# Performance work log

Measured on AMD Instinct MI355X. Metric: run time of the kernel, lower is better.

## Reference

```python
import jax, jax.numpy as jnp
import numpy as np

B, S, D, H = 4, 2048, 1024, 16
HD = D // H  # head_dim = 64


def setup_inputs() -> dict:
    key = jax.random.key(0)
    k1, k2, k3 = jax.random.split(key, 3)
    scale = 0.02
    return {
        "hidden_states": jax.random.normal(k1, (B, S, D), dtype=jnp.float32),
        "W_attn": jax.random.normal(k2, (D, 3 * D), dtype=jnp.float32) * scale,
        "b_attn": jnp.zeros((3 * D,), dtype=jnp.float32),
        "W_proj": jax.random.normal(k3, (D, D), dtype=jnp.float32) * scale,
        "b_proj": jnp.zeros((D,), dtype=jnp.float32),
    }


def reference(hidden_states, W_attn, b_attn, W_proj, b_proj):
    b, s, d = hidden_states.shape
    qkv = hidden_states @ W_attn + b_attn  # [B,S,3D]
    q, k, v = jnp.split(qkv, 3, axis=-1)
    # [B,S,D] -> [B,H,S,hd]
    def to_heads(x):
        return x.reshape(b, s, H, HD).transpose(0, 2, 1, 3)
    q, k, v = to_heads(q), to_heads(k), to_heads(v)
    scores = jnp.einsum("bhqd,bhkd->bhqk", q, k) / jnp.sqrt(jnp.float32(HD))
    causal = jnp.tril(jnp.ones((s, s), dtype=bool))  # [S,S]
    scores = jnp.where(causal[None, None], scores, jnp.float32(-jnp.inf))
    probs = jax.nn.softmax(scores, axis=-1)  # dropout p=0 -> identity (eval)
    out = jnp.einsum("bhqk,bhkd->bhqd", probs, v)  # [B,H,S,hd]
    out = out.transpose(0, 2, 1, 3).reshape(b, s, d)
    return out @ W_proj + b_proj
```

## Files before the change

kernel.cpp:

```cpp
#include <hip/hip_runtime.h>
#include <hip/hip_bf16.h>


typedef float f32x4 __attribute__((ext_vector_type(4)));
typedef __bf16 bf16x8 __attribute__((ext_vector_type(8)));
typedef unsigned short u16x8 __attribute__((ext_vector_type(8)));
typedef unsigned short u16x4 __attribute__((ext_vector_type(4)));

static constexpr int Sq = 2048, Dm = 1024, HD = 64, N3 = 3072;
static constexpr int Mrows = 4 * Sq;
static constexpr float SM_SCALE = 0.18033688011112042f;
static constexpr float SM_BIAS  = -11.541560327111707f;

__device__ __forceinline__ unsigned short f2bf(float f) {
  return __builtin_bit_cast(unsigned short, (__bf16)f);
}
__device__ __forceinline__ f32x4 mfma16(u16x8 a, u16x8 b, f32x4 c) {
  return __builtin_amdgcn_mfma_f32_16x16x32_bf16(
      __builtin_bit_cast(bf16x8, a), __builtin_bit_cast(bf16x8, b), c, 0, 0, 0);
}

__global__ __launch_bounds__(256) void cvt_k(
    const float* __restrict__ in, unsigned short* __restrict__ out, int n) {
  int stride = gridDim.x * 256 * 4;
  for (int i = (blockIdx.x * 256 + threadIdx.x) * 4; i < n; i += stride) {
    f32x4 v = *reinterpret_cast<const f32x4*>(&in[i]);
    u16x4 o;
    #pragma unroll
    for (int j = 0; j < 4; j++) o[j] = f2bf(v[j]);
    *reinterpret_cast<u16x4*>(&out[i]) = o;
  }
}

__global__ __launch_bounds__(256) void tcvt_k(
    const float* __restrict__ in, unsigned short* __restrict__ out,
    int R, int C) {
  __shared__ float tile[32][33];
  int c0 = blockIdx.x * 32, r0 = blockIdx.y * 32;
  int tx = threadIdx.x & 31, ty = threadIdx.x >> 5;
  #pragma unroll
  for (int i = 0; i < 32; i += 8)
    tile[ty + i][tx] = in[(size_t)(r0 + ty + i) * C + c0 + tx];
  __syncthreads();
  #pragma unroll
  for (int i = 0; i < 32; i += 8)
    out[(size_t)(c0 + ty + i) * R + r0 + tx] = f2bf(tile[tx][ty + i]);
}

template <bool OUT_F32>
__global__ __launch_bounds__(256) void gemm_bt(
    const unsigned short* __restrict__ A, const unsigned short* __restrict__ Bt,
    const float* __restrict__ bias, void* __restrict__ Cout,
    int Md, int Nd, int Kd) {
  __shared__ unsigned short Asm[128 * 32];
  __shared__ unsigned short Bsm[128 * 32];
  int t = threadIdx.x;
  int wave = t >> 6, lane = t & 63;
  int lrow = lane & 15, lq = lane >> 4;
  int wr = wave >> 1, wc = wave & 1;
  int bm = blockIdx.y * 128, bn = blockIdx.x * 128;
  f32x4 acc[4][4] = {};

  for (int k0 = 0; k0 < Kd; k0 += 32) {
    __syncthreads();
    #pragma unroll
    for (int c = 0; c < 2; c++) {
      int e = c * 2048 + t * 8;
      int row = e >> 5, col = e & 31;
      const unsigned short* ga = A + (size_t)(bm + row) * Kd + k0 + col;
      const unsigned short* gb = Bt + (size_t)(bn + row) * Kd + k0 + col;
      __builtin_amdgcn_global_load_lds(
          (const __attribute__((address_space(1))) void*)ga,
          (__attribute__((address_space(3))) void*)((char*)Asm + c * 4096 + wave * 1024),
          16, 0, 0);
      __builtin_amdgcn_global_load_lds(
          (const __attribute__((address_space(1))) void*)gb,
          (__attribute__((address_space(3))) void*)((char*)Bsm + c * 4096 + wave * 1024),
          16, 0, 0);
    }
    __syncthreads();

    u16x8 af[4], bfr[4];
    #pragma unroll
    for (int m = 0; m < 4; m++)
      af[m] = *reinterpret_cast<const u16x8*>(&Asm[(wr * 64 + m * 16 + lrow) * 32 + lq * 8]);
    #pragma unroll
    for (int n = 0; n < 4; n++)
      bfr[n] = *reinterpret_cast<const u16x8*>(&Bsm[(wc * 64 + n * 16 + lrow) * 32 + lq * 8]);
    #pragma unroll
    for (int m = 0; m < 4; m++)
      #pragma unroll
      for (int n = 0; n < 4; n++)
        acc[m][n] = mfma16(af[m], bfr[n], acc[m][n]);
  }

  #pragma unroll
  for (int n = 0; n < 4; n++) {
    int col = bn + wc * 64 + n * 16 + lrow;
    float bv = bias[col];
    #pragma unroll
    for (int m = 0; m < 4; m++) {
      #pragma unroll
      for (int j = 0; j < 4; j++) {
        int row = bm + wr * 64 + m * 16 + lq * 4 + j;
        if constexpr (OUT_F32)
          ((float*)Cout)[(size_t)row * Nd + col] = acc[m][n][j] + bv;
        else
          ((unsigned short*)Cout)[(size_t)row * Nd + col] = f2bf(acc[m][n][j] + bv);
      }
    }
  }
}

__global__ __launch_bounds__(256) void attn_k(
    const unsigned short* __restrict__ qkv,
    unsigned short* __restrict__ ao) {
  int bh = blockIdx.y;
  int b = bh >> 4, h = bh & 15;
  int t = threadIdx.x, wave = t >> 6, lane = t & 63;
  int lrow = lane & 15, lq = lane >> 4;

  __shared__ unsigned short Kl[2][64][72];
  __shared__ unsigned short Vt[2][64][72];
  __shared__ unsigned short Pl[4][16][72];

  const size_t base = (size_t)b * Sq * N3;
  const unsigned short* Kbase = qkv + base + Dm + h * HD;
  const unsigned short* Vbase = qkv + base + 2 * Dm + h * HD;

  int irow = t >> 2, icol = (t & 3) * 16;
  int vd = lane, vkb = wave;

  u16x8 kr0, kr1, vr0, vr1;
  auto prefetch = [&](int kv) {
    const unsigned short* kp = Kbase + (size_t)(kv + irow) * N3 + icol;
    kr0 = *reinterpret_cast<const u16x8*>(kp);
    kr1 = *reinterpret_cast<const u16x8*>(kp + 8);
    const unsigned short* vp = Vbase + (size_t)kv * N3 + vd;
    #pragma unroll
    for (int i = 0; i < 8; i++) {
      vr0[i] = vp[(size_t)(vkb * 8 + i) * N3];
      vr1[i] = vp[(size_t)(32 + vkb * 8 + i) * N3];
    }
  };

  #pragma unroll 1
  for (int pass = 0; pass < 2; ++pass) {
    int qb = pass ? (int)blockIdx.x : 15 - (int)blockIdx.x;
    int q0 = qb * 128;
    int ntiles = 2 * qb + 2;

    u16x8 qf[2][2];
    #pragma unroll
    for (int m = 0; m < 2; m++) {
      const unsigned short* qp =
          qkv + base + (size_t)(q0 + wave * 32 + m * 16 + lrow) * N3 + h * HD + lq * 8;
      qf[m][0] = *reinterpret_cast<const u16x8*>(qp);
      qf[m][1] = *reinterpret_cast<const u16x8*>(qp + 32);
    }

    float lrun[2][4] = {};
    f32x4 oacc[2][4] = {};

    prefetch(0);

    #pragma unroll 1
    for (int kt = 0; kt < ntiles; ++kt) {
      int kv = kt * 64, bsel = kt & 1;
      *reinterpret_cast<u16x8*>(&Kl[bsel][irow][icol]) = kr0;
      *reinterpret_cast<u16x8*>(&Kl[bsel][irow][icol + 8]) = kr1;
      *reinterpret_cast<u16x8*>(&Vt[bsel][vd][vkb * 8]) = vr0;
      *reinterpret_cast<u16x8*>(&Vt[bsel][vd][32 + vkb * 8]) = vr1;
      if (kt + 1 < ntiles) prefetch(kv + 64);
      __syncthreads();

      u16x8 kf0[4], kf1[4], vf0[4], vf1[4];
      #pragma unroll
      for (int ct = 0; ct < 4; ct++) {
        kf0[ct] = *reinterpret_cast<const u16x8*>(&Kl[bsel][ct * 16 + lrow][lq * 8]);
        kf1[ct] = *reinterpret_cast<const u16x8*>(&Kl[bsel][ct * 16 + lrow][32 + lq * 8]);
      }
      f32x4 sacc[2][4] = {};
      #pragma unroll
      for (int m = 0; m < 2; m++)
        #pragma unroll
        for (int ct = 0; ct < 4; ct++) {
          sacc[m][ct] = mfma16(qf[m][0], kf0[ct], sacc[m][ct]);
          sacc[m][ct] = mfma16(qf[m][1], kf1[ct], sacc[m][ct]);
        }
      #pragma unroll
      for (int ht = 0; ht < 4; ht++) {
        vf0[ht] = *reinterpret_cast<const u16x8*>(&Vt[bsel][ht * 16 + lrow][lq * 8]);
        vf1[ht] = *reinterpret_cast<const u16x8*>(&Vt[bsel][ht * 16 + lrow][32 + lq * 8]);
      }

      #pragma unroll
      for (int m = 0; m < 2; m++) {
        int rbase = q0 + wave * 32 + m * 16 + lq * 4;
        float p[4][4], rs[4] = {0.f, 0.f, 0.f, 0.f};
        #pragma unroll
        for (int ct = 0; ct < 4; ct++) {
          int colg = kv + ct * 16 + lrow;
          #pragma unroll
          for (int j = 0; j < 4; j++) {
            float e = exp2f(fmaf(sacc[m][ct][j], SM_SCALE, SM_BIAS));
            e = (colg <= rbase + j) ? e : 0.f;
            p[ct][j] = e;
            rs[j] += e;
          }
        }
        #pragma unroll
        for (int j = 0; j < 4; j++) {
          rs[j] += __shfl_xor(rs[j], 1);
          rs[j] += __shfl_xor(rs[j], 2);
          rs[j] += __shfl_xor(rs[j], 4);
          rs[j] += __shfl_xor(rs[j], 8);
          lrun[m][j] += rs[j];
        }

        #pragma unroll
        for (int ct = 0; ct < 4; ct++)
          #pragma unroll
          for (int j = 0; j < 4; j++)
            Pl[wave][lq * 4 + j][ct * 16 + lrow] = f2bf(p[ct][j]);

        u16x8 pa0 = *reinterpret_cast<const u16x8*>(&Pl[wave][lrow][lq * 8]);
        u16x8 pa1 = *reinterpret_cast<const u16x8*>(&Pl[wave][lrow][32 + lq * 8]);
        #pragma unroll
        for (int ht = 0; ht < 4; ht++) {
          oacc[m][ht] = mfma16(pa0, vf0[ht], oacc[m][ht]);
          oacc[m][ht] = mfma16(pa1, vf1[ht], oacc[m][ht]);
        }
      }
    }

    #pragma unroll
    for (int m = 0; m < 2; m++)
      #pragma unroll
      for (int ht = 0; ht < 4; ht++)
        #pragma unroll
        for (int j = 0; j < 4; j++) {
          int rg = q0 + wave * 32 + m * 16 + lq * 4 + j;
          float v = oacc[m][ht][j] / lrun[m][j];
          ao[(size_t)(b * Sq + rg) * Dm + h * HD + ht * 16 + lrow] = f2bf(v);
        }
  }
}

extern "C" void kernel_launch(void* const* d_in, const int* in_sizes, int n_in,
                              void* d_out, int out_size, void* d_ws, size_t ws_size,
                              hipStream_t stream) {
  const float* hs = (const float*)d_in[0];
  const float* Wa = (const float*)d_in[1];
  const float* ba = (const float*)d_in[2];
  const float* Wp = (const float*)d_in[3];
  const float* bp = (const float*)d_in[4];
  float* out = (float*)d_out;

  char* ws = (char*)d_ws;
  unsigned short* QKV = (unsigned short*)ws;
  unsigned short* WaT = (unsigned short*)(ws + 50331648);
  unsigned short* AO  = (unsigned short*)(ws + 50331648);
  unsigned short* WpT = (unsigned short*)ws;
  unsigned short* hsB = (unsigned short*)d_out;

  cvt_k<<<2048, 256, 0, stream>>>(hs, hsB, Mrows * Dm);
  tcvt_k<<<dim3(96, 32), 256, 0, stream>>>(Wa, WaT, 1024, 3072);
  gemm_bt<false><<<dim3(24, 64), 256, 0, stream>>>(hsB, WaT, ba, QKV, Mrows, N3, Dm);
  attn_k<<<dim3(8, 64), 256, 0, stream>>>(QKV, AO);
  tcvt_k<<<dim3(32, 32), 256, 0, stream>>>(Wp, WpT, 1024, 1024);
  gemm_bt<true><<<dim3(8, 64), 256, 0, stream>>>(AO, WpT, bp, out, Mrows, Dm, Dm);
}
```

Measured before the change: 232.9 us.

## Swizzle V-transpose LDS layout, defer row-sum shuffles, skip mask on full tiles

Three changes to the attention inner loop. An XOR swizzle on the transposed V tile in LDS is meant to cut bank conflicts on both the per-lane stores and the MFMA fragment reads. Row-sum lane shuffles move out of the key-tile loop: each lane keeps a partial sum and reduces once per pass. The causal mask compare is skipped for tiles lying entirely below the diagonal. Together these cut per-iteration shuffle and ALU work, at the cost of more complex LDS indexing.

After: 227.3 us. 2.4% less time.

```diff
diff --git a/kernel.cpp b/kernel.cpp
--- a/kernel.cpp
+++ b/kernel.cpp
@@ -130,6 +130,7 @@
 
   int irow = t >> 2, icol = (t & 3) * 16;
   int vd = lane, vkb = wave;
+  int vswW = ((vd >> 3) & 7) << 3;
 
   u16x8 kr0, kr1, vr0, vr1;
   auto prefetch = [&](int kv) {
@@ -169,8 +170,8 @@
       int kv = kt * 64, bsel = kt & 1;
       *reinterpret_cast<u16x8*>(&Kl[bsel][irow][icol]) = kr0;
       *reinterpret_cast<u16x8*>(&Kl[bsel][irow][icol + 8]) = kr1;
-      *reinterpret_cast<u16x8*>(&Vt[bsel][vd][vkb * 8]) = vr0;
-      *reinterpret_cast<u16x8*>(&Vt[bsel][vd][32 + vkb * 8]) = vr1;
+      *reinterpret_cast<u16x8*>(&Vt[bsel][vd][(vkb * 8) ^ vswW]) = vr0;
+      *reinterpret_cast<u16x8*>(&Vt[bsel][vd][(32 + vkb * 8) ^ vswW]) = vr1;
       if (kt + 1 < ntiles) prefetch(kv + 64);
       __syncthreads();
 
@@ -190,32 +191,27 @@
         }
       #pragma unroll
       for (int ht = 0; ht < 4; ht++) {
-        vf0[ht] = *reinterpret_cast<const u16x8*>(&Vt[bsel][ht * 16 + lrow][lq * 8]);
-        vf1[ht] = *reinterpret_cast<const u16x8*>(&Vt[bsel][ht * 16 + lrow][32 + lq * 8]);
+        int vsw = ((2 * ht + (lrow >> 3)) & 7) << 3;
+        vf0[ht] = *reinterpret_cast<const u16x8*>(&Vt[bsel][ht * 16 + lrow][(lq * 8) ^ vsw]);
+        vf1[ht] = *reinterpret_cast<const u16x8*>(&Vt[bsel][ht * 16 + lrow][(32 + lq * 8) ^ vsw]);
       }
 
       #pragma unroll
       for (int m = 0; m < 2; m++) {
-        int rbase = q0 + wave * 32 + m * 16 + lq * 4;
-        float p[4][4], rs[4] = {0.f, 0.f, 0.f, 0.f};
+        int rwm = q0 + wave * 32 + m * 16;
+        int rbase = rwm + lq * 4;
+        bool need_mask = kv + 63 > rwm;
+        float p[4][4];
         #pragma unroll
         for (int ct = 0; ct < 4; ct++) {
           int colg = kv + ct * 16 + lrow;
           #pragma unroll
           for (int j = 0; j < 4; j++) {
             float e = exp2f(fmaf(sacc[m][ct][j], SM_SCALE, SM_BIAS));
-            e = (colg <= rbase + j) ? e : 0.f;
+            if (need_mask) e = (colg <= rbase + j) ? e : 0.f;
             p[ct][j] = e;
-            rs[j] += e;
+            lrun[m][j] += e;
           }
-        }
-        #pragma unroll
-        for (int j = 0; j < 4; j++) {
-          rs[j] += __shfl_xor(rs[j], 1);
-          rs[j] += __shfl_xor(rs[j], 2);
-          rs[j] += __shfl_xor(rs[j], 4);
-          rs[j] += __shfl_xor(rs[j], 8);
-          lrun[m][j] += rs[j];
         }
 
         #pragma unroll
@@ -233,6 +229,18 @@
         }
       }
     }
+
+    #pragma unroll
+    for (int m = 0; m < 2; m++)
+      #pragma unroll
+      for (int j = 0; j < 4; j++) {
+        float r = lrun[m][j];
+        r += __shfl_xor(r, 1);
+        r += __shfl_xor(r, 2);
+        r += __shfl_xor(r, 4);
+        r += __shfl_xor(r, 8);
+        lrun[m][j] = r;
+      }
 
     #pragma unroll
     for (int m = 0; m < 2; m++)
```

## Transpose QK^T MFMA operands to keep row sums lane-local and vectorize P stores

Applied to the files above, without the earlier changes.

Swaps the A/B operands of the score MFMA so each lane holds scores for a single query row. The per-tile row-sum shuffles become one cross-lane reduction after the KV loop, and P can be written to LDS as packed 4-element vectors instead of scattered scalars. The causal mask is now applied only on tiles that cross the diagonal, and the final division uses a fast reciprocal. The layout change must stay consistent with the P/V MFMA, and the reciprocal is slightly less accurate.

Result: faster. 212.9 us (-8.6%).

```diff
diff --git a/kernel.cpp b/kernel.cpp
--- a/kernel.cpp
+++ b/kernel.cpp
@@ -159,7 +159,7 @@
       qf[m][1] = *reinterpret_cast<const u16x8*>(qp + 32);
     }
 
-    float lrun[2][4] = {};
+    float lrun[2] = {0.f, 0.f};
     f32x4 oacc[2][4] = {};
 
     prefetch(0);
@@ -185,8 +185,8 @@
       for (int m = 0; m < 2; m++)
         #pragma unroll
         for (int ct = 0; ct < 4; ct++) {
-          sacc[m][ct] = mfma16(qf[m][0], kf0[ct], sacc[m][ct]);
-          sacc[m][ct] = mfma16(qf[m][1], kf1[ct], sacc[m][ct]);
+          sacc[m][ct] = mfma16(kf0[ct], qf[m][0], sacc[m][ct]);
+          sacc[m][ct] = mfma16(kf1[ct], qf[m][1], sacc[m][ct]);
         }
       #pragma unroll
       for (int ht = 0; ht < 4; ht++) {
@@ -196,33 +196,28 @@
 
       #pragma unroll
       for (int m = 0; m < 2; m++) {
-        int rbase = q0 + wave * 32 + m * 16 + lq * 4;
-        float p[4][4], rs[4] = {0.f, 0.f, 0.f, 0.f};
+        int rwm = q0 + wave * 32 + m * 16;
+        bool need_mask = kv + 63 > rwm;
+        int dlim = rwm - kv + lrow;
+        float p[4][4];
         #pragma unroll
         for (int ct = 0; ct < 4; ct++) {
-          int colg = kv + ct * 16 + lrow;
           #pragma unroll
           for (int j = 0; j < 4; j++) {
             float e = exp2f(fmaf(sacc[m][ct][j], SM_SCALE, SM_BIAS));
-            e = (colg <= rbase + j) ? e : 0.f;
+            if (need_mask) e = (16 * ct + 4 * lq + j <= dlim) ? e : 0.f;
             p[ct][j] = e;
-            rs[j] += e;
+            lrun[m] += e;
           }
         }
-        #pragma unroll
-        for (int j = 0; j < 4; j++) {
-          rs[j] += __shfl_xor(rs[j], 1);
-          rs[j] += __shfl_xor(rs[j], 2);
-          rs[j] += __shfl_xor(rs[j], 4);
-          rs[j] += __shfl_xor(rs[j], 8);
-          lrun[m][j] += rs[j];
-        }
-
-        #pragma unroll
-        for (int ct = 0; ct < 4; ct++)
+
+        #pragma unroll
+        for (int ct = 0; ct < 4; ct++) {
+          u16x4 o;
           #pragma unroll
-          for (int j = 0; j < 4; j++)
-            Pl[wave][lq * 4 + j][ct * 16 + lrow] = f2bf(p[ct][j]);
+          for (int j = 0; j < 4; j++) o[j] = f2bf(p[ct][j]);
+          *reinterpret_cast<u16x4*>(&Pl[wave][lrow][16 * ct + 4 * lq]) = o;
+        }
 
         u16x8 pa0 = *reinterpret_cast<const u16x8*>(&Pl[wave][lrow][lq * 8]);
         u16x8 pa1 = *reinterpret_cast<const u16x8*>(&Pl[wave][lrow][32 + lq * 8]);
@@ -235,15 +230,28 @@
     }
 
     #pragma unroll
-    for (int m = 0; m < 2; m++)
+    for (int m = 0; m < 2; m++) {
+      float r = lrun[m];
+      r += __shfl_xor(r, 16);
+      r += __shfl_xor(r, 32);
+      lrun[m] = r;
+    }
+
+    #pragma unroll
+    for (int m = 0; m < 2; m++) {
+      float inv[4];
+      #pragma unroll
+      for (int j = 0; j < 4; j++)
+        inv[j] = __builtin_amdgcn_rcpf(__shfl(lrun[m], lq * 4 + j));
       #pragma unroll
       for (int ht = 0; ht < 4; ht++)
         #pragma unroll
         for (int j = 0; j < 4; j++) {
           int rg = q0 + wave * 32 + m * 16 + lq * 4 + j;
-          float v = oacc[m][ht][j] / lrun[m][j];
+          float v = oacc[m][ht][j] * inv[j];
           ao[(size_t)(b * Sq + rg) * Dm + h * HD + ht * 16 + lrow] = f2bf(v);
         }
+    }
   }
 }
 
```
